# Performance work log

Measured on AMD Instinct MI355X. Metric: run time of the kernel, lower is better.

## Reference

```python
import jax, jax.numpy as jnp
import numpy as np

D_MODEL = 2048
N_EXPERTS = 8
TOP_K = 2
FFN_HIDDEN = int(D_MODEL * 1.5)  # 3072, matches int(d_model*1.5)


def setup_inputs() -> dict:
    key = jax.random.key(0)
    k_x, k_r, k_g, k_u, k_d = jax.random.split(key, 5)
    B, L = 4, 4096
    s_in = 1.0 / np.sqrt(D_MODEL)
    s_hid = 1.0 / np.sqrt(FFN_HIDDEN)
    return {
        "x": jax.random.normal(k_x, (B, L, D_MODEL), dtype=jnp.float32),
        # nn.Linear weights are stored (out_features, in_features)
        "router_w": jax.random.uniform(k_r, (N_EXPERTS, D_MODEL), jnp.float32, -s_in, s_in),
        "gate_w": jax.random.uniform(k_g, (N_EXPERTS, FFN_HIDDEN, D_MODEL), jnp.float32, -s_in, s_in),
        "up_w": jax.random.uniform(k_u, (N_EXPERTS, FFN_HIDDEN, D_MODEL), jnp.float32, -s_in, s_in),
        "down_w": jax.random.uniform(k_d, (N_EXPERTS, D_MODEL, FFN_HIDDEN), jnp.float32, -s_hid, s_hid),
    }


def reference(x, router_w, gate_w, up_w, down_w):
    B, L, D = x.shape
    x_flat = x.reshape(-1, D)                                   # [N, D]

    router_logits = x_flat @ router_w.T                          # [N, E]
    router_probs = jax.nn.softmax(router_logits, axis=-1)
    top_k_probs, top_k_idx = jax.lax.top_k(router_probs, TOP_K)  # [N, K]
    top_k_probs = top_k_probs / jnp.sum(top_k_probs, axis=-1, keepdims=True)

    # combine[n, e] = sum_k top_k_probs[n,k] * (top_k_idx[n,k] == e)
    onehot = jax.nn.one_hot(top_k_idx, N_EXPERTS, dtype=x.dtype)  # [N, K, E]
    combine = jnp.einsum("nk,nke->ne", top_k_probs, onehot)       # [N, E]

    # Masked gather/scatter in the original == weight-0 tokens here; same math.
    output = jnp.zeros_like(x_flat)
    for e in range(N_EXPERTS):
        gate = jax.nn.silu(x_flat @ gate_w[e].T)                  # [N, H]
        up = x_flat @ up_w[e].T                                   # [N, H]
        expert_out = (gate * up) @ down_w[e].T                    # [N, D]
        output = output + combine[:, e:e + 1] * expert_out

    # dropout is identity in eval/reference mode
    return output.reshape(B, L, D)
```

## Files before the change

kernel.cpp:

```cpp
#include <hip/hip_runtime.h>
#include <hip/hip_bf16.h>
#include <cstdint>

#define N_TOK 16384
#define DMODEL 2048
#define FFH    3072
#define NGU    (2 * FFH)
#define NEXP   8
#define ATOT   32768

typedef __bf16 bf16;
typedef __attribute__((ext_vector_type(8))) __bf16 bf16x8;
typedef __attribute__((ext_vector_type(4))) __bf16 bf16x4;
typedef __attribute__((ext_vector_type(4))) float  f32x4;

__device__ __forceinline__ void gl_lds16(const bf16* g, void* l) {
  __builtin_amdgcn_global_load_lds(
      (const __attribute__((address_space(1))) void*)g,
      (__attribute__((address_space(3))) void*)l, 16, 0, 0);
}

__global__ void cvt_f32_bf16(const float* __restrict__ src, bf16* __restrict__ dst, long n4) {
  long i = (long)blockIdx.x * blockDim.x + threadIdx.x;
  if (i >= n4) return;
  const float4 v = ((const float4*)src)[i];
  bf16x4 o;
  o.x = (bf16)v.x; o.y = (bf16)v.y; o.z = (bf16)v.z; o.w = (bf16)v.w;
  ((bf16x4*)dst)[i] = o;
}

__global__ void cvt_guw(const float* __restrict__ gw, const float* __restrict__ uw,
                        bf16* __restrict__ guw) {
  const long i = (long)blockIdx.x * 256 + threadIdx.x;
  const int c8 = (int)(i & 255);
  const long rg = i >> 8;
  const int e = (int)(rg / NGU);
  const int ri = (int)(rg - (long)e * NGU);
  const int hb = ri >> 6, sub = ri & 63;
  const float* src = (sub < 32 ? gw : uw) + ((size_t)e * FFH + hb * 32 + (sub & 31)) * DMODEL + c8 * 8;
  const float4 v0 = ((const float4*)src)[0];
  const float4 v1 = ((const float4*)src)[1];
  bf16x8 o;
  o[0] = (bf16)v0.x; o[1] = (bf16)v0.y; o[2] = (bf16)v0.z; o[3] = (bf16)v0.w;
  o[4] = (bf16)v1.x; o[5] = (bf16)v1.y; o[6] = (bf16)v1.z; o[7] = (bf16)v1.w;
  *(bf16x8*)(guw + rg * DMODEL + c8 * 8) = o;
}

__global__ void router_k(const float* __restrict__ x, const float* __restrict__ rw,
                         int* __restrict__ tk_e, float* __restrict__ tk_w,
                         int* __restrict__ cnt) {
  const int wv = threadIdx.x >> 6, lane = threadIdx.x & 63;
  const int t = blockIdx.x * 4 + wv;
  const float* xr = x + (size_t)t * DMODEL;
  float acc[NEXP];
#pragma unroll
  for (int e = 0; e < NEXP; ++e) acc[e] = 0.f;
  for (int k = lane; k < DMODEL; k += 64) {
    const float xv = xr[k];
#pragma unroll
    for (int e = 0; e < NEXP; ++e) acc[e] = fmaf(xv, rw[e * DMODEL + k], acc[e]);
  }
#pragma unroll
  for (int e = 0; e < NEXP; ++e) {
#pragma unroll
    for (int o = 32; o; o >>= 1) acc[e] += __shfl_xor(acc[e], o, 64);
  }
  if (lane == 0) {
    int e0 = 0; float v0 = acc[0];
#pragma unroll
    for (int e = 1; e < NEXP; ++e) if (acc[e] > v0) { v0 = acc[e]; e0 = e; }
    int e1 = -1; float v1 = -1e30f;
#pragma unroll
    for (int e = 0; e < NEXP; ++e) if (e != e0 && acc[e] > v1) { v1 = acc[e]; e1 = e; }
    const float w0 = 1.f / (1.f + __expf(v1 - v0));
    tk_e[t * 2] = e0; tk_e[t * 2 + 1] = e1;
    tk_w[t * 2] = w0; tk_w[t * 2 + 1] = 1.f - w0;
    atomicAdd(&cnt[e0], 1); atomicAdd(&cnt[e1], 1);
  }
}

__global__ void offs_k(const int* __restrict__ cnt, int* __restrict__ offs) {
  if (threadIdx.x == 0) {
    int o = 0;
    for (int e = 0; e < NEXP; ++e) { offs[e] = o; o += cnt[e]; }
  }
}

__global__ void scatter_k(const int* __restrict__ tk_e, const float* __restrict__ tk_w,
                          const int* __restrict__ offs, int* __restrict__ cnt2,
                          int* __restrict__ tok_list, float* __restrict__ w_list,
                          int* __restrict__ aidx) {
  const int t = blockIdx.x * 256 + threadIdx.x;
  if (t >= N_TOK) return;
#pragma unroll
  for (int k = 0; k < 2; ++k) {
    const int e = tk_e[t * 2 + k];
    const int p = atomicAdd(&cnt2[e], 1);
    const int a = offs[e] + p;
    tok_list[a] = t;
    w_list[a] = tk_w[t * 2 + k];
    aidx[t * 2 + k] = a;
  }
}

template<int EPI>
__global__ __launch_bounds__(512, 2) void gemm_moe(
    const bf16* __restrict__ A, const bf16* __restrict__ B,
    bf16* __restrict__ hbuf, float* __restrict__ ybuf,
    const int* __restrict__ tok_list, const int* __restrict__ cnt,
    const int* __restrict__ offs) {
  constexpr int KD = EPI ? FFH : DMODEL;
  constexpr int NT = KD / 32;
  constexpr int BROWS = EPI ? DMODEL : NGU;

  const int e = blockIdx.z;
  const int cn = cnt[e];
  const int mbase = blockIdx.y * 256;
  if (mbase >= cn) return;
  const int offE = offs[e];
  const int nbase = blockIdx.x * 256;

  __shared__ char lds[98304];
  char* const ldsA = lds;
  char* const ldsB = lds + 49152;

  const int tid = threadIdx.x;
  const int wv = tid >> 6, lane = tid & 63;
  const int wr = wv >> 2, wc = wv & 3;

  const int sr = tid >> 2;
  const int swz8 = ((tid & 3) ^ ((tid >> 3) & 3)) * 8;
  const bf16* pA[2]; const bf16* pB[2];
  if (EPI == 0) {
    const int t0 = tok_list[offE + min(mbase + sr, cn - 1)];
    const int t1 = tok_list[offE + min(mbase + 128 + sr, cn - 1)];
    pA[0] = A + (size_t)t0 * KD + swz8;
    pA[1] = A + (size_t)t1 * KD + swz8;
  } else {
    const int a0 = offE + min(mbase + sr, cn - 1);
    const int a1 = offE + min(mbase + 128 + sr, cn - 1);
    pA[0] = A + (size_t)a0 * KD + swz8;
    pA[1] = A + (size_t)a1 * KD + swz8;
  }
  pB[0] = B + ((size_t)e * BROWS + nbase + sr) * KD + swz8;
  pB[1] = B + ((size_t)e * BROWS + nbase + 128 + sr) * KD + swz8;

  const int stageDst = wv * 1024;

  const int rswz = ((lane >> 4) ^ ((lane >> 1) & 3)) * 16;
  const int arow = (wr * 128 + (lane & 15)) * 64 + rswz;
  const int brow = (wc * 64 + (lane & 15)) * 64 + rswz;

  const f32x4 zero = {0.f, 0.f, 0.f, 0.f};
  f32x4 acc[8][4];
#pragma unroll
  for (int i = 0; i < 8; ++i)
#pragma unroll
    for (int j = 0; j < 4; ++j) acc[i][j] = zero;

  auto stage_half = [&](int buf, int q, int kt) {
    const int k8 = kt * 32;
    if (q < 2) gl_lds16(pA[q] + k8, ldsA + buf * 16384 + q * 8192 + stageDst);
    else       gl_lds16(pB[q - 2] + k8, ldsB + buf * 16384 + (q - 2) * 8192 + stageDst);
  };

#pragma unroll
  for (int q = 0; q < 4; ++q) stage_half(0, q, 0);
#pragma unroll
  for (int q = 0; q < 4; ++q) stage_half(1, q, 1);
  asm volatile("s_waitcnt vmcnt(4)" ::: "memory");
  __builtin_amdgcn_s_barrier();
  asm volatile("" ::: "memory");

  int cb = 0;
  for (int kt = 0; kt < NT; ++kt) {
    const int sb = (cb + 2 >= 3) ? cb - 1 : cb + 2;
    const char* cA = ldsA + cb * 16384;
    const char* cB = ldsB + cb * 16384;

    bf16x8 a[8], b[4];
#pragma unroll
    for (int i = 0; i < 4; ++i) {
      a[i] = *(const bf16x8*)(cA + i * 1024 + arow);
      b[i] = *(const bf16x8*)(cB + i * 1024 + brow);
    }
#pragma unroll
    for (int i = 4; i < 8; ++i) a[i] = *(const bf16x8*)(cA + i * 1024 + arow);

    if (kt + 2 < NT) { stage_half(sb, 0, kt + 2); stage_half(sb, 1, kt + 2); }

    __builtin_amdgcn_s_setprio(1);
#pragma unroll
    for (int nf = 0; nf < 4; ++nf)
#pragma unroll
      for (int mi = 0; mi < 4; ++mi)
        acc[mi][nf] = __builtin_amdgcn_mfma_f32_16x16x32_bf16(a[mi], b[nf], acc[mi][nf], 0, 0, 0);
    __builtin_amdgcn_s_setprio(0);

    if (kt + 2 < NT) { stage_half(sb, 2, kt + 2); stage_half(sb, 3, kt + 2); }

    __builtin_amdgcn_s_setprio(1);
#pragma unroll
    for (int nf = 0; nf < 4; ++nf)
#pragma unroll
      for (int mi = 4; mi < 8; ++mi)
        acc[mi][nf] = __builtin_amdgcn_mfma_f32_16x16x32_bf16(a[mi], b[nf], acc[mi][nf], 0, 0, 0);
    __builtin_amdgcn_s_setprio(0);

    if (kt + 2 < NT) { asm volatile("s_waitcnt vmcnt(4)" ::: "memory"); }
    else             { asm volatile("s_waitcnt vmcnt(0)" ::: "memory"); }
    asm volatile("" ::: "memory");
    __builtin_amdgcn_s_barrier();
    asm volatile("" ::: "memory");

    cb = (cb + 1 == 3) ? 0 : cb + 1;
  }

  const int col = lane & 15;
  const int rb = mbase + wr * 128 + (lane >> 4) * 4;
  if (EPI == 0) {
    const int hb32 = ((nbase + wc * 64) >> 6) * 32;
#pragma unroll
    for (int mi = 0; mi < 8; ++mi)
#pragma unroll
      for (int j = 0; j < 4; ++j) {
        const int row = rb + mi * 16 + j;
        if (row < cn) {
          bf16* hr = hbuf + (size_t)(offE + row) * FFH + hb32 + col;
#pragma unroll
          for (int k = 0; k < 2; ++k) {
            const float g = acc[mi][k][j], u = acc[mi][k + 2][j];
            hr[k * 16] = (bf16)(g / (1.f + __expf(-g)) * u);
          }
        }
      }
  } else {
#pragma unroll
    for (int mi = 0; mi < 8; ++mi)
#pragma unroll
      for (int j = 0; j < 4; ++j) {
        const int row = rb + mi * 16 + j;
        if (row < cn) {
          float* yr = ybuf + (size_t)(offE + row) * DMODEL + nbase + wc * 64 + col;
#pragma unroll
          for (int nf = 0; nf < 4; ++nf) yr[nf * 16] = acc[mi][nf][j];
        }
      }
  }
}

__global__ void combine_k(const float* __restrict__ ybuf, const int* __restrict__ aidx,
                          const float* __restrict__ tk_w, float* __restrict__ out) {
  const int i = blockIdx.x * 256 + threadIdx.x;
  const int t = i >> 9, c = i & 511;
  const int a0 = aidx[t * 2], a1 = aidx[t * 2 + 1];
  const float w0 = tk_w[t * 2], w1 = tk_w[t * 2 + 1];
  const float4 v0 = ((const float4*)(ybuf + (size_t)a0 * DMODEL))[c];
  const float4 v1 = ((const float4*)(ybuf + (size_t)a1 * DMODEL))[c];
  float4 o;
  o.x = w0 * v0.x + w1 * v1.x;
  o.y = w0 * v0.y + w1 * v1.y;
  o.z = w0 * v0.z + w1 * v1.z;
  o.w = w0 * v0.w + w1 * v1.w;
  ((float4*)(out + (size_t)t * DMODEL))[c] = o;
}

extern "C" void kernel_launch(void* const* d_in, const int* in_sizes, int n_in,
                              void* d_out, int out_size, void* d_ws, size_t ws_size,
                              hipStream_t stream) {
  const float* x  = (const float*)d_in[0];
  const float* rw = (const float*)d_in[1];
  const float* gw = (const float*)d_in[2];
  const float* uw = (const float*)d_in[3];
  const float* dw = (const float*)d_in[4];
  float* out = (float*)d_out;

  char* ws = (char*)d_ws;
  size_t o = 0;
  auto alloc = [&](size_t bytes) {
    void* p = ws + o;
    o = (o + bytes + 255) & ~(size_t)255;
    return p;
  };

  const size_t guw_bytes  = (size_t)NEXP * NGU * DMODEL * 2;
  const size_t ybuf_bytes = (size_t)(ATOT + 256) * DMODEL * 4;
  bf16*  xb       = (bf16*)alloc((size_t)N_TOK * DMODEL * 2);
  void*  uni      = alloc(ybuf_bytes > guw_bytes ? ybuf_bytes : guw_bytes);
  bf16*  guw      = (bf16*)uni;
  float* ybuf     = (float*)uni;
  bf16*  dwb      = (bf16*)alloc((size_t)NEXP * DMODEL * FFH * 2);
  bf16*  hbuf     = (bf16*)alloc((size_t)(ATOT + 256) * FFH * 2);
  int*   tok_list = (int*)alloc((ATOT + 256) * 4);
  float* w_list   = (float*)alloc((ATOT + 256) * 4);
  int*   tk_e     = (int*)alloc((size_t)N_TOK * 2 * 4);
  float* tk_w     = (float*)alloc((size_t)N_TOK * 2 * 4);
  int*   aidx     = (int*)alloc((size_t)N_TOK * 2 * 4);
  int*   cnt      = (int*)alloc(64);
  int*   offs     = (int*)alloc(64);
  int*   cnt2     = (int*)alloc(64);

  hipMemsetAsync(cnt, 0, 64, stream);
  hipMemsetAsync(cnt2, 0, 64, stream);

  {
    long n4 = (long)N_TOK * DMODEL / 4;
    cvt_f32_bf16<<<(unsigned)(n4 / 256), 256, 0, stream>>>(x, xb, n4);
  }
  cvt_guw<<<(unsigned)((long)NEXP * NGU * DMODEL / 8 / 256), 256, 0, stream>>>(gw, uw, guw);
  {
    long n4 = (long)NEXP * DMODEL * FFH / 4;
    cvt_f32_bf16<<<(unsigned)(n4 / 256), 256, 0, stream>>>(dw, dwb, n4);
  }

  router_k<<<N_TOK / 4, 256, 0, stream>>>(x, rw, tk_e, tk_w, cnt);
  offs_k<<<1, 64, 0, stream>>>(cnt, offs);
  scatter_k<<<N_TOK / 256, 256, 0, stream>>>(tk_e, tk_w, offs, cnt2, tok_list, w_list, aidx);

  gemm_moe<0><<<dim3(NGU / 256, 64, NEXP), 512, 0, stream>>>(
      xb, guw, hbuf, nullptr, tok_list, cnt, offs);
  gemm_moe<1><<<dim3(DMODEL / 256, 64, NEXP), 512, 0, stream>>>(
      hbuf, dwb, nullptr, ybuf, tok_list, cnt, offs);

  combine_k<<<N_TOK * 512 / 256, 256, 0, stream>>>(ybuf, aidx, tk_w, out);
}
```

Baseline: 1.999 ms.

## Fuse x conversion into router, bf16 weighted ybuf, XCD-aware block remap

The router kernel now writes the bf16 copy of x while it reads x for the routing logits, so the separate conversion pass over x goes away. The down-projection GEMM multiplies each output row by its routing weight and stores ybuf as bf16, which halves ybuf traffic and turns the combine step into a plain sum. Block indices are remapped so consecutive blocks are spread across the 8 XCDs, aiming for better L2 locality per die. The cost is extra bf16 rounding of the expert outputs before they are summed.

Measured after the change: 1.966 ms. Within noise of the previous version (-1.6%).

```diff
diff --git a/kernel.cpp b/kernel.cpp
--- a/kernel.cpp
+++ b/kernel.cpp
@@ -47,18 +47,28 @@
 }
 
 __global__ void router_k(const float* __restrict__ x, const float* __restrict__ rw,
+                         bf16* __restrict__ xb,
                          int* __restrict__ tk_e, float* __restrict__ tk_w,
                          int* __restrict__ cnt) {
   const int wv = threadIdx.x >> 6, lane = threadIdx.x & 63;
   const int t = blockIdx.x * 4 + wv;
-  const float* xr = x + (size_t)t * DMODEL;
+  const float4* xr = (const float4*)(x + (size_t)t * DMODEL);
+  bf16x4* xbr = (bf16x4*)(xb + (size_t)t * DMODEL);
   float acc[NEXP];
 #pragma unroll
   for (int e = 0; e < NEXP; ++e) acc[e] = 0.f;
-  for (int k = lane; k < DMODEL; k += 64) {
-    const float xv = xr[k];
-#pragma unroll
-    for (int e = 0; e < NEXP; ++e) acc[e] = fmaf(xv, rw[e * DMODEL + k], acc[e]);
+#pragma unroll
+  for (int it = 0; it < DMODEL / 4 / 64; ++it) {
+    const int idx = lane + it * 64;
+    const float4 v = xr[idx];
+    bf16x4 o;
+    o.x = (bf16)v.x; o.y = (bf16)v.y; o.z = (bf16)v.z; o.w = (bf16)v.w;
+    xbr[idx] = o;
+#pragma unroll
+    for (int e = 0; e < NEXP; ++e) {
+      const float4 w = ((const float4*)(rw + e * DMODEL))[idx];
+      acc[e] = fmaf(v.x, w.x, fmaf(v.y, w.y, fmaf(v.z, w.z, fmaf(v.w, w.w, acc[e]))));
+    }
   }
 #pragma unroll
   for (int e = 0; e < NEXP; ++e) {
@@ -106,19 +116,24 @@
 template<int EPI>
 __global__ __launch_bounds__(512, 2) void gemm_moe(
     const bf16* __restrict__ A, const bf16* __restrict__ B,
-    bf16* __restrict__ hbuf, float* __restrict__ ybuf,
-    const int* __restrict__ tok_list, const int* __restrict__ cnt,
-    const int* __restrict__ offs) {
+    bf16* __restrict__ hbuf, bf16* __restrict__ ybuf,
+    const int* __restrict__ tok_list, const float* __restrict__ w_list,
+    const int* __restrict__ cnt, const int* __restrict__ offs) {
   constexpr int KD = EPI ? FFH : DMODEL;
   constexpr int NT = KD / 32;
   constexpr int BROWS = EPI ? DMODEL : NGU;
 
   const int e = blockIdx.z;
   const int cn = cnt[e];
-  const int mbase = blockIdx.y * 256;
+  const int gy = gridDim.y;
+  const int flat = blockIdx.x + gridDim.x * blockIdx.y;
+  const int q = (gridDim.x * gy) >> 3;
+  const int flat2 = (flat & 7) * q + (flat >> 3);
+  const int nbt = flat2 / gy;
+  const int mbase = (flat2 - nbt * gy) * 256;
   if (mbase >= cn) return;
   const int offE = offs[e];
-  const int nbase = blockIdx.x * 256;
+  const int nbase = nbt * 256;
 
   __shared__ char lds[98304];
   char* const ldsA = lds;
@@ -158,16 +173,16 @@
 #pragma unroll
     for (int j = 0; j < 4; ++j) acc[i][j] = zero;
 
-  auto stage_half = [&](int buf, int q, int kt) {
+  auto stage_half = [&](int buf, int qh, int kt) {
     const int k8 = kt * 32;
-    if (q < 2) gl_lds16(pA[q] + k8, ldsA + buf * 16384 + q * 8192 + stageDst);
-    else       gl_lds16(pB[q - 2] + k8, ldsB + buf * 16384 + (q - 2) * 8192 + stageDst);
+    if (qh < 2) gl_lds16(pA[qh] + k8, ldsA + buf * 16384 + qh * 8192 + stageDst);
+    else        gl_lds16(pB[qh - 2] + k8, ldsB + buf * 16384 + (qh - 2) * 8192 + stageDst);
   };
 
 #pragma unroll
-  for (int q = 0; q < 4; ++q) stage_half(0, q, 0);
-#pragma unroll
-  for (int q = 0; q < 4; ++q) stage_half(1, q, 1);
+  for (int qh = 0; qh < 4; ++qh) stage_half(0, qh, 0);
+#pragma unroll
+  for (int qh = 0; qh < 4; ++qh) stage_half(1, qh, 1);
   asm volatile("s_waitcnt vmcnt(4)" ::: "memory");
   __builtin_amdgcn_s_barrier();
   asm volatile("" ::: "memory");
@@ -241,28 +256,33 @@
       for (int j = 0; j < 4; ++j) {
         const int row = rb + mi * 16 + j;
         if (row < cn) {
-          float* yr = ybuf + (size_t)(offE + row) * DMODEL + nbase + wc * 64 + col;
-#pragma unroll
-          for (int nf = 0; nf < 4; ++nf) yr[nf * 16] = acc[mi][nf][j];
+          const float wg = w_list[offE + row];
+          bf16* yr = ybuf + (size_t)(offE + row) * DMODEL + nbase + wc * 64 + col;
+#pragma unroll
+          for (int nf = 0; nf < 4; ++nf) yr[nf * 16] = (bf16)(wg * acc[mi][nf][j]);
         }
       }
   }
 }
 
-__global__ void combine_k(const float* __restrict__ ybuf, const int* __restrict__ aidx,
-                          const float* __restrict__ tk_w, float* __restrict__ out) {
+__global__ void combine_k(const bf16* __restrict__ ybuf, const int* __restrict__ aidx,
+                          float* __restrict__ out) {
   const int i = blockIdx.x * 256 + threadIdx.x;
-  const int t = i >> 9, c = i & 511;
+  const int t = i >> 8, c = i & 255;
   const int a0 = aidx[t * 2], a1 = aidx[t * 2 + 1];
-  const float w0 = tk_w[t * 2], w1 = tk_w[t * 2 + 1];
-  const float4 v0 = ((const float4*)(ybuf + (size_t)a0 * DMODEL))[c];
-  const float4 v1 = ((const float4*)(ybuf + (size_t)a1 * DMODEL))[c];
-  float4 o;
-  o.x = w0 * v0.x + w1 * v1.x;
-  o.y = w0 * v0.y + w1 * v1.y;
-  o.z = w0 * v0.z + w1 * v1.z;
-  o.w = w0 * v0.w + w1 * v1.w;
-  ((float4*)(out + (size_t)t * DMODEL))[c] = o;
+  const bf16x8 v0 = ((const bf16x8*)(ybuf + (size_t)a0 * DMODEL))[c];
+  const bf16x8 v1 = ((const bf16x8*)(ybuf + (size_t)a1 * DMODEL))[c];
+  float4 o0, o1;
+  o0.x = (float)v0[0] + (float)v1[0];
+  o0.y = (float)v0[1] + (float)v1[1];
+  o0.z = (float)v0[2] + (float)v1[2];
+  o0.w = (float)v0[3] + (float)v1[3];
+  o1.x = (float)v0[4] + (float)v1[4];
+  o1.y = (float)v0[5] + (float)v1[5];
+  o1.z = (float)v0[6] + (float)v1[6];
+  o1.w = (float)v0[7] + (float)v1[7];
+  float4* op = (float4*)(out + (size_t)t * DMODEL + c * 8);
+  op[0] = o0; op[1] = o1;
 }
 
 extern "C" void kernel_launch(void* const* d_in, const int* in_sizes, int n_in,
@@ -284,11 +304,11 @@
   };
 
   const size_t guw_bytes  = (size_t)NEXP * NGU * DMODEL * 2;
-  const size_t ybuf_bytes = (size_t)(ATOT + 256) * DMODEL * 4;
+  const size_t ybuf_bytes = (size_t)(ATOT + 256) * DMODEL * 2;
   bf16*  xb       = (bf16*)alloc((size_t)N_TOK * DMODEL * 2);
-  void*  uni      = alloc(ybuf_bytes > guw_bytes ? ybuf_bytes : guw_bytes);
+  void*  uni      = alloc(guw_bytes > ybuf_bytes ? guw_bytes : ybuf_bytes);
   bf16*  guw      = (bf16*)uni;
-  float* ybuf     = (float*)uni;
+  bf16*  ybuf     = (bf16*)uni;
   bf16*  dwb      = (bf16*)alloc((size_t)NEXP * DMODEL * FFH * 2);
   bf16*  hbuf     = (bf16*)alloc((size_t)(ATOT + 256) * FFH * 2);
   int*   tok_list = (int*)alloc((ATOT + 256) * 4);
@@ -303,24 +323,20 @@
   hipMemsetAsync(cnt, 0, 64, stream);
   hipMemsetAsync(cnt2, 0, 64, stream);
 
-  {
-    long n4 = (long)N_TOK * DMODEL / 4;
-    cvt_f32_bf16<<<(unsigned)(n4 / 256), 256, 0, stream>>>(x, xb, n4);
-  }
+  router_k<<<N_TOK / 4, 256, 0, stream>>>(x, rw, xb, tk_e, tk_w, cnt);
+  offs_k<<<1, 64, 0, stream>>>(cnt, offs);
+  scatter_k<<<N_TOK / 256, 256, 0, stream>>>(tk_e, tk_w, offs, cnt2, tok_list, w_list, aidx);
+
   cvt_guw<<<(unsigned)((long)NEXP * NGU * DMODEL / 8 / 256), 256, 0, stream>>>(gw, uw, guw);
   {
     long n4 = (long)NEXP * DMODEL * FFH / 4;
     cvt_f32_bf16<<<(unsigned)(n4 / 256), 256, 0, stream>>>(dw, dwb, n4);
   }
 
-  router_k<<<N_TOK / 4, 256, 0, stream>>>(x, rw, tk_e, tk_w, cnt);
-  offs_k<<<1, 64, 0, stream>>>(cnt, offs);
-  scatter_k<<<N_TOK / 256, 256, 0, stream>>>(tk_e, tk_w, offs, cnt2, tok_list, w_list, aidx);
-
   gemm_moe<0><<<dim3(NGU / 256, 64, NEXP), 512, 0, stream>>>(
-      xb, guw, hbuf, nullptr, tok_list, cnt, offs);
+      xb, guw, hbuf, nullptr, tok_list, w_list, cnt, offs);
   gemm_moe<1><<<dim3(DMODEL / 256, 64, NEXP), 512, 0, stream>>>(
-      hbuf, dwb, nullptr, ybuf, tok_list, cnt, offs);
-
-  combine_k<<<N_TOK * 512 / 256, 256, 0, stream>>>(ybuf, aidx, tk_w, out);
-}
+      hbuf, dwb, nullptr, ybuf, tok_list, w_list, cnt, offs);
+
+  combine_k<<<N_TOK, 256, 0, stream>>>(ybuf, aidx, out);
+}
```
